# Kernel optimization log

Hardware: AMD Instinct MI355X
Metric: run time of the kernel (lower is better)

## Reference

```python
import jax, jax.numpy as jnp
import numpy as np

N, D, B, H = 131072, 512, 512, 8  # nodes, hidden_dim, graphs, heads


def setup_inputs() -> dict:
    key = jax.random.key(0)
    ks = jax.random.split(key, 4)
    x = jax.random.normal(ks[0], (N, D), jnp.float32)
    # sorted segment ids; every graph nonempty (matches torch batch.max()+1 semantics)
    batch = jnp.sort(jnp.arange(N, dtype=jnp.int32) % B)
    query = jax.random.normal(ks[1], (D,), jnp.float32)          # nn.Parameter(randn(1,1,D))
    W_in = jax.random.normal(ks[2], (3 * D, D), jnp.float32) / np.sqrt(D)  # MHA in_proj_weight
    b_in = jnp.zeros((3 * D,), jnp.float32)
    W_out = jax.random.normal(ks[3], (D, D), jnp.float32) / np.sqrt(D)     # MHA out_proj
    b_out = jnp.zeros((D,), jnp.float32)
    return {"x": x, "batch": batch, "num_graphs": B, "query": query,
            "W_in": W_in, "b_in": b_in, "W_out": W_out, "b_out": b_out}


def reference(x, batch, num_graphs, query, W_in, b_in, W_out, b_out):
    # Fused ragged single-query multihead attention pooling (eval mode: dropout off).
    D = x.shape[1]
    dh = D // H
    scale = 1.0 / np.sqrt(dh)
    # q/k/v projections (torch MHA packed in_proj: rows [0:D]=q, [D:2D]=k, [2D:3D]=v)
    q = ((query @ W_in[:D].T + b_in[:D]) * scale).reshape(H, dh)       # [H, dh], shared across graphs
    k = (x @ W_in[D:2 * D].T + b_in[D:2 * D]).reshape(-1, H, dh)       # [N, H, dh]
    v = (x @ W_in[2 * D:].T + b_in[2 * D:]).reshape(-1, H, dh)         # [N, H, dh]
    scores = jnp.einsum('nhd,hd->nh', k, q)                             # [N, H]
    # segment (per-graph) softmax over nodes
    smax = jax.ops.segment_max(scores, batch, num_segments=num_graphs)  # [B, H]
    e = jnp.exp(scores - smax[batch])
    denom = jax.ops.segment_sum(e, batch, num_segments=num_graphs)      # [B, H]
    p = e / denom[batch]                                                # [N, H]
    pooled = jax.ops.segment_sum(p[:, :, None] * v, batch, num_segments=num_graphs)  # [B, H, dh]
    return pooled.reshape(num_graphs, D) @ W_out.T + b_out              # [B, D]
```

## Files before the change

### kernel.cpp

```cpp
#include <hip/hip_runtime.h>
#include <math.h>

#define NHEAD 8

template <int CTRL>
__device__ __forceinline__ float dpp_add(float v) {
    int r = __builtin_amdgcn_mov_dpp(__float_as_int(v), CTRL, 0xF, 0xF, false);
    return v + __int_as_float(r);
}

__global__ void __launch_bounds__(256) k_setup(const float* __restrict__ query,
                                               const float* __restrict__ W_in,
                                               const float* __restrict__ b_in,
                                               const int* __restrict__ batch,
                                               float* __restrict__ wsc,
                                               int* __restrict__ seg_start,
                                               int* __restrict__ seg_end,
                                               int N, float scale) {
    const int g = blockIdx.x, t = threadIdx.x;
    if (g < 16) {
        __shared__ float qs4[64][4];
        __shared__ float qs[64];
        const int h = g >> 1, half = g & 1;
        {
            const int d = t & 63, qtr = t >> 6;
            const int row = h * 64 + d;
            const float4* wq = reinterpret_cast<const float4*>(W_in + (size_t)row * 512 + qtr * 128);
            const float4* qv = reinterpret_cast<const float4*>(query + qtr * 128);
            float a = 0.f;
#pragma unroll 8
            for (int i = 0; i < 32; ++i) {
                float4 w = wq[i], q = qv[i];
                a += w.x * q.x + w.y * q.y + w.z * q.z + w.w * q.w;
            }
            qs4[d][qtr] = a;
        }
        __syncthreads();
        if (t < 64) {
            const float s = qs4[t][0] + qs4[t][1] + qs4[t][2] + qs4[t][3];
            qs[t] = (s + b_in[h * 64 + t]) * scale;
        }
        __syncthreads();
        const int i = half * 256 + t;
        const float* Wk = W_in + (size_t)512 * 512;
        float a = 0.f;
#pragma unroll 8
        for (int d = 0; d < 64; ++d)
            a += qs[d] * Wk[(size_t)(h * 64 + d) * 512 + i];
        wsc[h * 512 + i] = a;
    } else {
        const int stride = (gridDim.x - 16) * 256;
        for (int n = (g - 16) * 256 + t; n < N; n += stride) {
            int b = batch[n];
            if (n == 0 || batch[n - 1] != b) seg_start[b] = n;
            if (n == N - 1 || batch[n + 1] != b) seg_end[b] = n + 1;
        }
    }
}

__global__ void __launch_bounds__(256, 2) k_fused1(const float* __restrict__ x,
                                                   const float* __restrict__ wsc,
                                                   const int* __restrict__ seg_start,
                                                   const int* __restrict__ seg_end,
                                                   float* __restrict__ xp) {
    __shared__ float mrg[4][64][64];
    __shared__ float dsum[4][NHEAD];
    const int b = blockIdx.x, t = threadIdx.x;
    const int lane = t & 63, w = t >> 6;
    const int s0 = seg_start[b], s1 = seg_end[b];
    const int len = s1 - s0;
    const int clen = (len + 3) >> 2;
    const int r0 = s0 + w * clen;
    const int r1 = min(s1, r0 + clen);

    float4 w0[NHEAD], w1[NHEAD];
#pragma unroll
    for (int h = 0; h < NHEAD; ++h) {
        w0[h] = *reinterpret_cast<const float4*>(wsc + h * 512 + lane * 8);
        w1[h] = *reinterpret_cast<const float4*>(wsc + h * 512 + lane * 8 + 4);
    }

    float acc[NHEAD][8];
#pragma unroll
    for (int h = 0; h < NHEAD; ++h)
#pragma unroll
        for (int j = 0; j < 8; ++j) acc[h][j] = 0.f;
    float dacc[NHEAD];
#pragma unroll
    for (int h = 0; h < NHEAD; ++h) dacc[h] = 0.f;

    float4 a0, a1, n0, n1;
    const float* xl = x + lane * 8;
    if (r0 < r1) {
        a0 = *reinterpret_cast<const float4*>(xl + (size_t)r0 * 512);
        a1 = *reinterpret_cast<const float4*>(xl + (size_t)r0 * 512 + 4);
    }
    if (r0 + 1 < r1) {
        n0 = *reinterpret_cast<const float4*>(xl + (size_t)(r0 + 1) * 512);
        n1 = *reinterpret_cast<const float4*>(xl + (size_t)(r0 + 1) * 512 + 4);
    }

    for (int r = r0; r < r1; ++r) {
        const float4 c0 = a0, c1 = a1;
        a0 = n0; a1 = n1;
        if (r + 2 < r1) {
            n0 = *reinterpret_cast<const float4*>(xl + (size_t)(r + 2) * 512);
            n1 = *reinterpret_cast<const float4*>(xl + (size_t)(r + 2) * 512 + 4);
        }
        float e[NHEAD];
#pragma unroll
        for (int h = 0; h < NHEAD; ++h) {
            float d = c0.x * w0[h].x + c0.y * w0[h].y + c0.z * w0[h].z + c0.w * w0[h].w +
                      c1.x * w1[h].x + c1.y * w1[h].y + c1.z * w1[h].z + c1.w * w1[h].w;
            d = dpp_add<0xB1>(d);
            d = dpp_add<0x4E>(d);
            d = dpp_add<0x141>(d);
            d = dpp_add<0x140>(d);
            d += __shfl_xor(d, 16, 64);
            d += __shfl_xor(d, 32, 64);
            e[h] = __expf(d);
        }
#pragma unroll
        for (int h = 0; h < NHEAD; ++h) {
            dacc[h] += e[h];
            acc[h][0] += e[h] * c0.x; acc[h][1] += e[h] * c0.y;
            acc[h][2] += e[h] * c0.z; acc[h][3] += e[h] * c0.w;
            acc[h][4] += e[h] * c1.x; acc[h][5] += e[h] * c1.y;
            acc[h][6] += e[h] * c1.z; acc[h][7] += e[h] * c1.w;
        }
    }

#pragma unroll
    for (int h = 0; h < NHEAD; ++h)
#pragma unroll
        for (int j = 0; j < 8; ++j)
            mrg[w][h * 8 + j][lane] = acc[h][j];
    if (lane == 0) {
#pragma unroll
        for (int h = 0; h < NHEAD; ++h) dsum[w][h] = dacc[h];
    }
    __syncthreads();

    {
        const int c0i = 2 * t;
        const int lsrc = c0i >> 3, slot = c0i & 7;
        float* xpb = xp + (size_t)b * (NHEAD * 512);
#pragma unroll
        for (int h = 0; h < NHEAD; ++h) {
            const float den = dsum[0][h] + dsum[1][h] + dsum[2][h] + dsum[3][h];
            const float rl = 1.f / den;
            float num0 = 0.f, num1 = 0.f;
#pragma unroll
            for (int g = 0; g < 4; ++g) {
                num0 += mrg[g][h * 8 + slot][lsrc];
                num1 += mrg[g][h * 8 + slot + 1][lsrc];
            }
            float2 o;
            o.x = num0 * rl;
            o.y = num1 * rl;
            *reinterpret_cast<float2*>(xpb + (size_t)h * 512 + c0i) = o;
        }
    }
}

__global__ void __launch_bounds__(256) k_gemm_tn4w(const float* __restrict__ A, int lda, int zA,
                                                   const float* __restrict__ Bm, int ldb, int zB,
                                                   const float* __restrict__ bias, int zBias,
                                                   float* __restrict__ C, int ldc, int zC, int K) {
    __shared__ float As[4][32][36];
    __shared__ float Bs[4][32][36];
    __shared__ float red[4][32][32];
    const int z = blockIdx.z;
    A += (size_t)z * zA;
    Bm += (size_t)z * zB;
    bias += (size_t)z * zBias;
    C += (size_t)z * zC;
    const int m0 = blockIdx.x * 32, n0 = blockIdx.y * 32;
    const int t = threadIdx.x;
    const int w = t >> 6, lane = t & 63;
    const int row = lane >> 1, c0 = (lane & 1) * 16;
    const int ty = lane >> 3, tx = lane & 7;
    const int Kw = K >> 2;
    const int kw0 = w * Kw;
    float c[4][4];
#pragma unroll
    for (int i = 0; i < 4; ++i)
#pragma unroll
        for (int j = 0; j < 4; ++j) c[i][j] = 0.f;

    for (int kt = 0; kt < Kw; kt += 32) {
        const int k0 = kw0 + kt;
        const float* Ar = A + (size_t)(m0 + row) * lda + k0 + c0;
        const float* Br = Bm + (size_t)(n0 + row) * ldb + k0 + c0;
        float4 a4[4], b4[4];
#pragma unroll
        for (int j = 0; j < 4; ++j) {
            a4[j] = *reinterpret_cast<const float4*>(Ar + j * 4);
            b4[j] = *reinterpret_cast<const float4*>(Br + j * 4);
        }
#pragma unroll
        for (int j = 0; j < 4; ++j) {
            As[w][c0 + j * 4 + 0][row] = a4[j].x;
            As[w][c0 + j * 4 + 1][row] = a4[j].y;
            As[w][c0 + j * 4 + 2][row] = a4[j].z;
            As[w][c0 + j * 4 + 3][row] = a4[j].w;
            Bs[w][c0 + j * 4 + 0][row] = b4[j].x;
            Bs[w][c0 + j * 4 + 1][row] = b4[j].y;
            Bs[w][c0 + j * 4 + 2][row] = b4[j].z;
            Bs[w][c0 + j * 4 + 3][row] = b4[j].w;
        }
#pragma unroll
        for (int kk = 0; kk < 32; ++kk) {
            float4 av = *reinterpret_cast<const float4*>(&As[w][kk][ty * 4]);
            float4 bv = *reinterpret_cast<const float4*>(&Bs[w][kk][tx * 4]);
            c[0][0] += av.x * bv.x; c[0][1] += av.x * bv.y; c[0][2] += av.x * bv.z; c[0][3] += av.x * bv.w;
            c[1][0] += av.y * bv.x; c[1][1] += av.y * bv.y; c[1][2] += av.y * bv.z; c[1][3] += av.y * bv.w;
            c[2][0] += av.z * bv.x; c[2][1] += av.z * bv.y; c[2][2] += av.z * bv.z; c[2][3] += av.z * bv.w;
            c[3][0] += av.w * bv.x; c[3][1] += av.w * bv.y; c[3][2] += av.w * bv.z; c[3][3] += av.w * bv.w;
        }
    }
#pragma unroll
    for (int i = 0; i < 4; ++i)
#pragma unroll
        for (int j = 0; j < 4; ++j) red[w][ty * 4 + i][tx * 4 + j] = c[i][j];
    __syncthreads();
    const int r = t >> 3, cc = (t & 7) * 4;
    float4 s = {0.f, 0.f, 0.f, 0.f};
#pragma unroll
    for (int g = 0; g < 4; ++g) {
        const float4 v = *reinterpret_cast<const float4*>(&red[g][r][cc]);
        s.x += v.x; s.y += v.y; s.z += v.z; s.w += v.w;
    }
    const float4 bv4 = *reinterpret_cast<const float4*>(bias + n0 + cc);
    float4 o = {s.x + bv4.x, s.y + bv4.y, s.z + bv4.z, s.w + bv4.w};
    *reinterpret_cast<float4*>(C + (size_t)(m0 + r) * ldc + n0 + cc) = o;
}

extern "C" void kernel_launch(void* const* d_in, const int* in_sizes, int n_in,
                              void* d_out, int out_size, void* d_ws, size_t ws_size,
                              hipStream_t stream) {
    const float* x     = (const float*)d_in[0];
    const int*   batch = (const int*)d_in[1];
    const float* query = (const float*)d_in[3];
    const float* W_in  = (const float*)d_in[4];
    const float* b_in  = (const float*)d_in[5];
    const float* W_out = (const float*)d_in[6];
    const float* b_out = (const float*)d_in[7];
    float* out = (float*)d_out;

    const int D = in_sizes[3];
    const int N = in_sizes[0] / D;
    const int B = out_size / D;
    const int dh = D / NHEAD;
    const float scale = 1.0f / sqrtf((float)dh);

    float* wsf       = (float*)d_ws;
    float* wsc       = wsf;
    float* xp        = wsc + NHEAD * 512;
    float* pooled    = xp + (size_t)B * NHEAD * 512;
    int*   seg_start = (int*)(pooled + (size_t)B * 512);
    int*   seg_end   = seg_start + B;

    k_setup<<<16 + 256, 256, 0, stream>>>(query, W_in, b_in, batch, wsc,
                                          seg_start, seg_end, N, scale);

    k_fused1<<<B, 256, 0, stream>>>(x, wsc, seg_start, seg_end, xp);

    k_gemm_tn4w<<<dim3(B / 32, dh / 32, NHEAD), 256, 0, stream>>>(
        xp, NHEAD * 512, 512,
        W_in + (size_t)2 * D * D, D, dh * D,
        b_in + 2 * D, dh,
        pooled, D, dh, D);

    k_gemm_tn4w<<<dim3(B / 32, D / 32, 1), 256, 0, stream>>>(
        pooled, D, 0,
        W_out, D, 0,
        b_out, 0,
        out, D, 0, D);
}
```

Before: 105.5 us.

## Process two rows per iteration, deepen prefetch, use permlane swaps for reductions

The main streaming loop now handles two x rows per iteration and keeps three row pairs of loads in flight instead of one row ahead. The cross-row wave reductions replace the ds_bpermute-based __shfl_xor steps with v_permlane16/32_swap inline asm. The aim is more memory-level parallelism and independent reduction chains to hide latency, plus removing LDS round-trips from the reductions. The cost is higher register pressure from the extra prefetch buffers and doubled score arrays. The asm volatile with s_nop padding may also limit how the compiler schedules instructions.

```diff
diff --git a/kernel.cpp b/kernel.cpp
--- a/kernel.cpp
+++ b/kernel.cpp
@@ -7,6 +7,37 @@
 __device__ __forceinline__ float dpp_add(float v) {
     int r = __builtin_amdgcn_mov_dpp(__float_as_int(v), CTRL, 0xF, 0xF, false);
     return v + __int_as_float(r);
+}
+
+__device__ __forceinline__ float swap16_add(float v) {
+    int a = __float_as_int(v);
+    int b;
+    asm volatile("v_mov_b32 %1, %0\n\t"
+                 "s_nop 1\n\t"
+                 "v_permlane16_swap_b32 %0, %1\n\t"
+                 "s_nop 1"
+                 : "+v"(a), "=&v"(b));
+    return __int_as_float(a) + __int_as_float(b);
+}
+__device__ __forceinline__ float swap32_add(float v) {
+    int a = __float_as_int(v);
+    int b;
+    asm volatile("v_mov_b32 %1, %0\n\t"
+                 "s_nop 1\n\t"
+                 "v_permlane32_swap_b32 %0, %1\n\t"
+                 "s_nop 1"
+                 : "+v"(a), "=&v"(b));
+    return __int_as_float(a) + __int_as_float(b);
+}
+
+__device__ __forceinline__ float wave_allsum(float v) {
+    v = dpp_add<0xB1>(v);
+    v = dpp_add<0x4E>(v);
+    v = dpp_add<0x141>(v);
+    v = dpp_add<0x140>(v);
+    v = swap16_add(v);
+    v = swap32_add(v);
+    return v;
 }
 
 __global__ void __launch_bounds__(256) k_setup(const float* __restrict__ query,
@@ -89,46 +120,57 @@
 #pragma unroll
     for (int h = 0; h < NHEAD; ++h) dacc[h] = 0.f;
 
-    float4 a0, a1, n0, n1;
     const float* xl = x + lane * 8;
-    if (r0 < r1) {
-        a0 = *reinterpret_cast<const float4*>(xl + (size_t)r0 * 512);
-        a1 = *reinterpret_cast<const float4*>(xl + (size_t)r0 * 512 + 4);
-    }
-    if (r0 + 1 < r1) {
-        n0 = *reinterpret_cast<const float4*>(xl + (size_t)(r0 + 1) * 512);
-        n1 = *reinterpret_cast<const float4*>(xl + (size_t)(r0 + 1) * 512 + 4);
-    }
-
-    for (int r = r0; r < r1; ++r) {
-        const float4 c0 = a0, c1 = a1;
-        a0 = n0; a1 = n1;
-        if (r + 2 < r1) {
-            n0 = *reinterpret_cast<const float4*>(xl + (size_t)(r + 2) * 512);
-            n1 = *reinterpret_cast<const float4*>(xl + (size_t)(r + 2) * 512 + 4);
-        }
-        float e[NHEAD];
+#define LD0(r) (*reinterpret_cast<const float4*>(xl + (size_t)(r) * 512))
+#define LD1(r) (*reinterpret_cast<const float4*>(xl + (size_t)(r) * 512 + 4))
+
+    float4 cA0, cA1, cB0, cB1, nA0, nA1, nB0, nB1, mA0, mA1, mB0, mB1;
+    if (r0 + 0 < r1) { cA0 = LD0(r0 + 0); cA1 = LD1(r0 + 0); }
+    if (r0 + 1 < r1) { cB0 = LD0(r0 + 1); cB1 = LD1(r0 + 1); }
+    if (r0 + 2 < r1) { nA0 = LD0(r0 + 2); nA1 = LD1(r0 + 2); }
+    if (r0 + 3 < r1) { nB0 = LD0(r0 + 3); nB1 = LD1(r0 + 3); }
+    if (r0 + 4 < r1) { mA0 = LD0(r0 + 4); mA1 = LD1(r0 + 4); }
+    if (r0 + 5 < r1) { mB0 = LD0(r0 + 5); mB1 = LD1(r0 + 5); }
+
+    for (int r = r0; r < r1; r += 2) {
+        const float4 a0 = cA0, a1 = cA1, b0 = cB0, b1 = cB1;
+        cA0 = nA0; cA1 = nA1; cB0 = nB0; cB1 = nB1;
+        nA0 = mA0; nA1 = mA1; nB0 = mB0; nB1 = mB1;
+        if (r + 6 < r1) { mA0 = LD0(r + 6); mA1 = LD1(r + 6); }
+        if (r + 7 < r1) { mB0 = LD0(r + 7); mB1 = LD1(r + 7); }
+
+        const bool hasB = (r + 1 < r1);
+        float eA[NHEAD], eB[NHEAD];
 #pragma unroll
         for (int h = 0; h < NHEAD; ++h) {
-            float d = c0.x * w0[h].x + c0.y * w0[h].y + c0.z * w0[h].z + c0.w * w0[h].w +
-                      c1.x * w1[h].x + c1.y * w1[h].y + c1.z * w1[h].z + c1.w * w1[h].w;
-            d = dpp_add<0xB1>(d);
-            d = dpp_add<0x4E>(d);
-            d = dpp_add<0x141>(d);
-            d = dpp_add<0x140>(d);
-            d += __shfl_xor(d, 16, 64);
-            d += __shfl_xor(d, 32, 64);
-            e[h] = __expf(d);
+            float dA = a0.x * w0[h].x + a0.y * w0[h].y + a0.z * w0[h].z + a0.w * w0[h].w +
+                       a1.x * w1[h].x + a1.y * w1[h].y + a1.z * w1[h].z + a1.w * w1[h].w;
+            float dB = b0.x * w0[h].x + b0.y * w0[h].y + b0.z * w0[h].z + b0.w * w0[h].w +
+                       b1.x * w1[h].x + b1.y * w1[h].y + b1.z * w1[h].z + b1.w * w1[h].w;
+            eA[h] = __expf(wave_allsum(dA));
+            eB[h] = __expf(wave_allsum(dB));
         }
 #pragma unroll
         for (int h = 0; h < NHEAD; ++h) {
-            dacc[h] += e[h];
-            acc[h][0] += e[h] * c0.x; acc[h][1] += e[h] * c0.y;
-            acc[h][2] += e[h] * c0.z; acc[h][3] += e[h] * c0.w;
-            acc[h][4] += e[h] * c1.x; acc[h][5] += e[h] * c1.y;
-            acc[h][6] += e[h] * c1.z; acc[h][7] += e[h] * c1.w;
-        }
-    }
+            dacc[h] += eA[h];
+            acc[h][0] += eA[h] * a0.x; acc[h][1] += eA[h] * a0.y;
+            acc[h][2] += eA[h] * a0.z; acc[h][3] += eA[h] * a0.w;
+            acc[h][4] += eA[h] * a1.x; acc[h][5] += eA[h] * a1.y;
+            acc[h][6] += eA[h] * a1.z; acc[h][7] += eA[h] * a1.w;
+        }
+        if (hasB) {
+#pragma unroll
+            for (int h = 0; h < NHEAD; ++h) {
+                dacc[h] += eB[h];
+                acc[h][0] += eB[h] * b0.x; acc[h][1] += eB[h] * b0.y;
+                acc[h][2] += eB[h] * b0.z; acc[h][3] += eB[h] * b0.w;
+                acc[h][4] += eB[h] * b1.x; acc[h][5] += eB[h] * b1.y;
+                acc[h][6] += eB[h] * b1.z; acc[h][7] += eB[h] * b1.w;
+            }
+        }
+    }
+#undef LD0
+#undef LD1
 
 #pragma unroll
     for (int h = 0; h < NHEAD; ++h)
```

Result: slower. 109.4 us (+3.7%).
